# Kernel tuning notes

Hardware: AMD Instinct MI355X
Metric: run time of the kernel (lower is better)

The kernel has to match this reference:

```python
import jax, jax.numpy as jnp
import numpy as np

B, S, H = 2, 2048, 2048
NH, HD = 16, 128


def rotate_half(x):
    x1, x2 = x[..., : x.shape[-1] // 2], x[..., x.shape[-1] // 2 :]
    return jnp.concatenate((-x2, x1), axis=-1)


def setup_inputs() -> dict:
    key = jax.random.key(0)
    ks = jax.random.split(key, 8)
    return {
        "hidden": jax.random.normal(ks[0], (B, S, H), dtype=jnp.float32),
        "cos": jax.random.uniform(ks[1], (S, HD), dtype=jnp.float32),
        "sin": jax.random.uniform(ks[2], (S, HD), dtype=jnp.float32),
        "attention_mask": jnp.zeros((B, 1, S, S), dtype=jnp.float32),
        "Wq": jax.random.normal(ks[3], (H, H), dtype=jnp.float32) * 0.02,
        "Wk": jax.random.normal(ks[4], (H, H), dtype=jnp.float32) * 0.02,
        "Wv": jax.random.normal(ks[5], (H, H), dtype=jnp.float32) * 0.02,
        "Wo": jax.random.normal(ks[6], (H, H), dtype=jnp.float32) * 0.02,
    }


def reference(hidden, cos, sin, attention_mask, Wq, Wk, Wv, Wo):
    b, s, h = hidden.shape
    # torch Linear: y = x @ W.T ; reshape to [B, NH, S, HD]
    def proj(W):
        return (hidden @ W.T).reshape(b, s, NH, HD).transpose(0, 2, 1, 3)

    q, k, v = proj(Wq), proj(Wk), proj(Wv)
    c = cos[None, None, :, :]  # [1,1,S,HD]
    si = sin[None, None, :, :]
    q = q * c + rotate_half(q) * si
    k = k * c + rotate_half(k) * si
    scores = jnp.einsum("bhqd,bhkd->bhqk", q, k) / jnp.sqrt(jnp.float32(HD))
    scores = scores + attention_mask
    attn = jax.nn.softmax(scores.astype(jnp.float32), axis=-1).astype(q.dtype)
    out = jnp.einsum("bhqk,bhkd->bhqd", attn, v)
    out = out.transpose(0, 2, 1, 3).reshape(b, s, h)
    return out @ Wo.T
```

## Files before the change

### kernel.cpp

```cpp
#include <hip/hip_runtime.h>
#include <hip/hip_bf16.h>
#include <math.h>

#define SEQ 2048
#define HID 2048
#define NHEAD 16
#define HDIM 128
#define LDK 4096

typedef __bf16 bf16_t;
typedef __bf16 bf16x2 __attribute__((ext_vector_type(2)));
typedef __bf16 bf16x4_t __attribute__((ext_vector_type(4)));
typedef __bf16 bf16x8 __attribute__((ext_vector_type(8)));
typedef float f32x4 __attribute__((ext_vector_type(4)));
typedef float f32x16 __attribute__((ext_vector_type(16)));
typedef unsigned u32x4 __attribute__((ext_vector_type(4)));

#define MFMA16(a, b, c) __builtin_amdgcn_mfma_f32_16x16x32_bf16(a, b, c, 0, 0, 0)
#define MFMA32(a, b, c) __builtin_amdgcn_mfma_f32_32x32x16_bf16(a, b, c, 0, 0, 0)
#define GLOAD_LDS(g, l) \
  __builtin_amdgcn_global_load_lds((const __attribute__((address_space(1))) void*)(g), \
                                   (__attribute__((address_space(3))) void*)(l), 16, 0, 0)

static __device__ inline unsigned pk2(float lo, float hi) {
  bf16x2 t; t[0] = (bf16_t)lo; t[1] = (bf16_t)hi;
  return __builtin_bit_cast(unsigned, t);
}

static __device__ inline bf16x8 pack_slice(const float* p, int hi) {
  unsigned A1 = pk2(p[0], p[1]);
  unsigned A2 = pk2(p[2], p[3]);
  unsigned B1 = pk2(p[4], p[5]);
  unsigned B2 = pk2(p[6], p[7]);
  unsigned A1s = __shfl_xor(A1, 32, 64);
  unsigned A2s = __shfl_xor(A2, 32, 64);
  unsigned B1s = __shfl_xor(B1, 32, 64);
  unsigned B2s = __shfl_xor(B2, 32, 64);
  unsigned w0 = hi ? B1s : A1;
  unsigned w1 = hi ? B2s : A2;
  unsigned w2 = hi ? B1 : A1s;
  unsigned w3 = hi ? B2 : A2s;
  u32x4 W = {w0, w1, w2, w3};
  return __builtin_bit_cast(bf16x8, W);
}

__global__ void cast_hidden(const float* __restrict__ in, bf16_t* __restrict__ out) {
  int i = blockIdx.x * 256 + threadIdx.x;
  float4 v = ((const float4*)in)[i];
  bf16x4_t b;
  b[0] = (bf16_t)v.x; b[1] = (bf16_t)v.y; b[2] = (bf16_t)v.z; b[3] = (bf16_t)v.w;
  ((bf16x4_t*)out)[i] = b;
}

__global__ void cast_weights(const float* __restrict__ a, const float* __restrict__ b,
                             const float* __restrict__ c, const float* __restrict__ d,
                             bf16_t* __restrict__ out) {
  const float* srcs[4] = {a, b, c, d};
  const float* src = srcs[blockIdx.y];
  bf16_t* dst = out + (size_t)blockIdx.y * (HID * HID);
  int i = blockIdx.x * 256 + threadIdx.x;
  float4 v = ((const float4*)src)[i];
  bf16x4_t o;
  o[0] = (bf16_t)v.x; o[1] = (bf16_t)v.y; o[2] = (bf16_t)v.z; o[3] = (bf16_t)v.w;
  ((bf16x4_t*)dst)[i] = o;
}

__global__ __launch_bounds__(512, 2) void gemm256(
    const bf16_t* __restrict__ A, const bf16_t* __restrict__ Bw,
    bf16_t* __restrict__ Cb, float* __restrict__ Cf, int M, int N, int K) {
  __shared__ char smem[131072];
  const int tid = threadIdx.x, lane = tid & 63, wid = tid >> 6;
  const int wr = wid >> 2, wc = wid & 3;
  const int lr = lane & 15, lg = lane >> 4;
  const int xcd = blockIdx.x & 7, l = blockIdx.x >> 3;
  const int brow = (xcd >> 2) * 8 + (l >> 2);
  const int bcol = (xcd & 3) * 4 + (l & 3);
  const int NT = K >> 6;

  const bf16_t* Ab = A + (size_t)(brow * 256) * K;
  const bf16_t* Bb = Bw + (size_t)(bcol * 256) * K;

  f32x4 acc[8][4] = {};
  bf16x8 af[4], bfr[4];
  const int swz = (lg ^ ((lr >> 1) & 3)) << 4;

#define STAGE_HALF(t_, op, kh)                                                        \
  {                                                                                   \
    int tt = (t_) < NT ? (t_) : NT - 1;                                               \
    const bf16_t* gsrc = (op) ? Bb : Ab;                                              \
    char* ldst = smem + (tt & 1) * 65536 + (op) * 32768 + (kh) * 16384;               \
    _Pragma("unroll") for (int is = 0; is < 2; ++is) {                                \
      int p = tid + is * 512;                                                         \
      int row = p >> 2, ch = p & 3;                                                   \
      GLOAD_LDS(gsrc + (size_t)row * K + tt * 64 + (kh) * 32 +                        \
                    ((ch ^ ((row >> 1) & 3)) * 8),                                    \
                ldst + p * 16);                                                       \
    }                                                                                 \
  }

#define PHASE(cb, kh, mh, LOADB, STAGECALL, VM)                                       \
  {                                                                                   \
    _Pragma("unroll") for (int mf = 0; mf < 4; ++mf) {                                \
      int row = wr * 128 + (mh) * 64 + mf * 16 + lr;                                  \
      af[mf] = *(const bf16x8*)(smem + (cb) * 65536 + (kh) * 16384 + row * 64 + swz); \
    }                                                                                 \
    if (LOADB) {                                                                      \
      _Pragma("unroll") for (int nf = 0; nf < 4; ++nf) {                              \
        int row = wc * 64 + nf * 16 + lr;                                             \
        bfr[nf] = *(const bf16x8*)(smem + (cb) * 65536 + 32768 + (kh) * 16384 +       \
                                   row * 64 + swz);                                   \
      }                                                                               \
    }                                                                                 \
    STAGECALL;                                                                        \
    __builtin_amdgcn_s_barrier();                                                     \
    asm volatile("s_waitcnt lgkmcnt(0)" ::: "memory");                                \
    __builtin_amdgcn_sched_barrier(0);                                                \
    __builtin_amdgcn_s_setprio(1);                                                    \
    _Pragma("unroll") for (int mf = 0; mf < 4; ++mf)                                  \
      _Pragma("unroll") for (int nf = 0; nf < 4; ++nf)                                \
        acc[(mh) * 4 + mf][nf] = MFMA16(af[mf], bfr[nf], acc[(mh) * 4 + mf][nf]);     \
    __builtin_amdgcn_s_setprio(0);                                                    \
    if (VM) { asm volatile("s_waitcnt vmcnt(6)" ::: "memory"); }                      \
    __builtin_amdgcn_s_barrier();                                                     \
    __builtin_amdgcn_sched_barrier(0);                                                \
  }

  STAGE_HALF(0, 1, 0); STAGE_HALF(0, 0, 0); STAGE_HALF(0, 1, 1); STAGE_HALF(0, 0, 1);
  STAGE_HALF(1, 1, 0); STAGE_HALF(1, 0, 0); STAGE_HALF(1, 1, 1);
  asm volatile("s_waitcnt vmcnt(6)" ::: "memory");
  __builtin_amdgcn_s_barrier();
  __builtin_amdgcn_sched_barrier(0);

  const int NI = NT >> 1;
  for (int i = 0; i < NI; ++i) {
    const int t2 = 2 * i;
    PHASE(0, 0, 0, 1, STAGE_HALF(t2 + 1, 0, 1), 0);
    PHASE(0, 0, 1, 0, STAGE_HALF(t2 + 2, 1, 0), 0);
    PHASE(0, 1, 0, 1, STAGE_HALF(t2 + 2, 0, 0), 0);
    PHASE(0, 1, 1, 0, STAGE_HALF(t2 + 2, 1, 1), 1);
    PHASE(1, 0, 0, 1, STAGE_HALF(t2 + 2, 0, 1), 0);
    PHASE(1, 0, 1, 0, STAGE_HALF(t2 + 3, 1, 0), 0);
    PHASE(1, 1, 0, 1, STAGE_HALF(t2 + 3, 0, 0), 0);
    PHASE(1, 1, 1, 0, STAGE_HALF(t2 + 3, 1, 1), 1);
  }
#undef PHASE
#undef STAGE_HALF

#pragma unroll
  for (int mi = 0; mi < 8; ++mi)
#pragma unroll
    for (int nf = 0; nf < 4; ++nf)
#pragma unroll
      for (int r = 0; r < 4; ++r) {
        int row = brow * 256 + wr * 128 + (mi >> 2) * 64 + (mi & 3) * 16 + lg * 4 + r;
        int col = bcol * 256 + wc * 64 + nf * 16 + lr;
        float v = acc[mi][nf][r];
        if (Cf) Cf[(size_t)row * N + col] = v;
        else    Cb[(size_t)row * N + col] = (bf16_t)v;
      }
}

__global__ __launch_bounds__(256, 3) void gemm_bt(
    const bf16_t* __restrict__ A, const bf16_t* __restrict__ Bw,
    bf16_t* __restrict__ Cb, float* __restrict__ Cf,
    int M, int N, int K) {
  __shared__ bf16_t As[2][128 * 32];
  __shared__ bf16_t Bs[2][128 * 32];
  const int tid = threadIdx.x;
  const int lane = tid & 63, wid = tid >> 6;
  const int wr = wid >> 1, wc = wid & 1;
  const int lr = lane & 15, lg = lane >> 4;
  const int nwg = gridDim.x;
  const int lid = (blockIdx.x & 7) * (nwg >> 3) + (blockIdx.x >> 3);
  const int nbc = N >> 7;
  const int brow = lid / nbc, bcol = lid % nbc;

  f32x4 acc[4][4] = {};
  const int swz = lg ^ ((lr >> 1) & 3);

  const int srow = tid >> 2, sch = tid & 3;
#define GSTAGE(k0, bb)                                                                   \
  {                                                                                      \
    _Pragma("unroll") for (int is = 0; is < 2; ++is) {                                   \
      int row = srow + is * 64;                                                          \
      int g = (sch ^ ((row >> 1) & 3)) * 8;                                              \
      GLOAD_LDS(A + (size_t)(brow * 128 + row) * K + (k0) + g,                           \
                &As[bb][(row * 4 + sch) * 8]);                                           \
      GLOAD_LDS(Bw + (size_t)(bcol * 128 + row) * K + (k0) + g,                          \
                &Bs[bb][(row * 4 + sch) * 8]);                                           \
    }                                                                                    \
  }

  GSTAGE(0, 0);
  __syncthreads();

  const int nt = K / 32;
  for (int t = 0; t < nt; ++t) {
    const int cb = t & 1;
    if (t + 1 < nt) GSTAGE((t + 1) * 32, cb ^ 1);
    bf16x8 af[4], bfr[4];
#pragma unroll
    for (int m = 0; m < 4; ++m)
      af[m] = *(const bf16x8*)(&As[cb][(wr * 64 + m * 16 + lr) * 32 + swz * 8]);
#pragma unroll
    for (int n = 0; n < 4; ++n)
      bfr[n] = *(const bf16x8*)(&Bs[cb][(wc * 64 + n * 16 + lr) * 32 + swz * 8]);
#pragma unroll
    for (int m = 0; m < 4; ++m)
#pragma unroll
      for (int n = 0; n < 4; ++n)
        acc[m][n] = MFMA16(af[m], bfr[n], acc[m][n]);
    __syncthreads();
  }
#undef GSTAGE

#pragma unroll
  for (int m = 0; m < 4; ++m)
#pragma unroll
    for (int n = 0; n < 4; ++n)
#pragma unroll
      for (int r = 0; r < 4; ++r) {
        int row = brow * 128 + wr * 64 + m * 16 + lg * 4 + r;
        int col = bcol * 128 + wc * 64 + n * 16 + lr;
        float v = acc[m][n][r];
        if (Cf) Cf[(size_t)row * N + col] = v;
        else    Cb[(size_t)row * N + col] = (bf16_t)v;
      }
}

__global__ void rope_qk(bf16_t* __restrict__ QK,
                        const float* __restrict__ cost, const float* __restrict__ sint) {
  const float SCALE = 0.08838834764831845f;
  int idx = blockIdx.x * 256 + threadIdx.x;
  int d8 = idx & 7;
  int t = idx >> 3;
  int h = t & 15;
  int row = t >> 4;
  int s = row & (SEQ - 1);
  size_t base = (size_t)row * LDK + h * HDIM;
  const float4* cp = (const float4*)(cost + s * HDIM);
  const float4* sp = (const float4*)(sint + s * HDIM);
  float4 c0a = cp[d8 * 2], c0b = cp[d8 * 2 + 1];
  float4 c1a = cp[16 + d8 * 2], c1b = cp[16 + d8 * 2 + 1];
  float4 s0a = sp[d8 * 2], s0b = sp[d8 * 2 + 1];
  float4 s1a = sp[16 + d8 * 2], s1b = sp[16 + d8 * 2 + 1];
  float c0[8] = {c0a.x, c0a.y, c0a.z, c0a.w, c0b.x, c0b.y, c0b.z, c0b.w};
  float c1[8] = {c1a.x, c1a.y, c1a.z, c1a.w, c1b.x, c1b.y, c1b.z, c1b.w};
  float s0[8] = {s0a.x, s0a.y, s0a.z, s0a.w, s0b.x, s0b.y, s0b.z, s0b.w};
  float s1[8] = {s1a.x, s1a.y, s1a.z, s1a.w, s1b.x, s1b.y, s1b.z, s1b.w};

  bf16_t* Q = QK;
  bf16_t* K = QK + 2048;
  bf16x8 qlo = *(bf16x8*)(Q + base + d8 * 8);
  bf16x8 qhi = *(bf16x8*)(Q + base + 64 + d8 * 8);
  bf16x8 klo = *(bf16x8*)(K + base + d8 * 8);
  bf16x8 khi = *(bf16x8*)(K + base + 64 + d8 * 8);
  bf16x8 qlo2, qhi2, klo2, khi2;
#pragma unroll
  for (int j = 0; j < 8; ++j) {
    float q0 = (float)qlo[j], q1 = (float)qhi[j];
    qlo2[j] = (bf16_t)((q0 * c0[j] - q1 * s0[j]) * SCALE);
    qhi2[j] = (bf16_t)((q1 * c1[j] + q0 * s1[j]) * SCALE);
    float k0 = (float)klo[j], k1 = (float)khi[j];
    klo2[j] = (bf16_t)(k0 * c0[j] - k1 * s0[j]);
    khi2[j] = (bf16_t)(k1 * c1[j] + k0 * s1[j]);
  }
  *(bf16x8*)(Q + base + d8 * 8) = qlo2;
  *(bf16x8*)(Q + base + 64 + d8 * 8) = qhi2;
  *(bf16x8*)(K + base + d8 * 8) = klo2;
  *(bf16x8*)(K + base + 64 + d8 * 8) = khi2;
}

__global__ void transpose_v(const bf16_t* __restrict__ Vf, bf16_t* __restrict__ Vt) {
  __shared__ bf16_t t[32][33];
  int tx = threadIdx.x & 31, ty = threadIdx.x >> 5;
  int r0 = blockIdx.y * 32, c0 = blockIdx.x * 32;
#pragma unroll
  for (int j = 0; j < 4; ++j)
    t[ty + j * 8][tx] = Vf[(size_t)(r0 + ty + j * 8) * HID + c0 + tx];
  __syncthreads();
#pragma unroll
  for (int j = 0; j < 4; ++j) {
    int c = c0 + ty + j * 8;
    int r = r0 + tx;
    int h = c >> 7, d = c & 127, b = r >> 11, s = r & (SEQ - 1);
    Vt[(((size_t)(b * NHEAD + h)) * HDIM + d) * SEQ + s] = t[tx][ty + j * 8];
  }
}

__global__ void mask_pack(const float* __restrict__ m, bf16_t* __restrict__ mp) {
  __shared__ float t[32][33];
  int tx = threadIdx.x & 31, ty = threadIdx.x >> 5;
  int q0 = blockIdx.x * 32, k0 = blockIdx.y * 32;
  const float* mb = m + (size_t)blockIdx.z * SEQ * SEQ;
#pragma unroll
  for (int j = 0; j < 4; ++j)
    t[ty + j * 8][tx] = mb[(size_t)(q0 + ty + j * 8) * SEQ + k0 + tx];
  __syncthreads();
  int r = tx & 15, hi = tx >> 4;
  int kl = (r & 3) + 8 * (r >> 2) + 4 * hi;
  bf16_t* ob = mp + ((size_t)(blockIdx.z * 64 + blockIdx.y) * 2048 + q0) * 32;
#pragma unroll
  for (int j = 0; j < 4; ++j) {
    int qloc = ty + j * 8;
    ob[(size_t)qloc * 32 + tx] = (bf16_t)t[qloc][kl];
  }
}

__global__ __launch_bounds__(256, 1) void flash_fwd(
    const bf16_t* __restrict__ Qf, const bf16_t* __restrict__ Kf,
    const bf16_t* __restrict__ Vt, const bf16_t* __restrict__ maskP,
    bf16_t* __restrict__ AO) {
  __shared__ char smem[131072];
  char* KsB = smem;
  char* VsB = smem + 65536;
  const int tid = threadIdx.x, lane = tid & 63, wid = tid >> 6;
  const int q32 = lane & 31, hi = lane >> 5;

  const int x = blockIdx.x;
  const int bh = x & 31, qt = x >> 5;
  const int b = bh >> 4, h = bh & 15;
  const int qg0 = qt * 256 + wid * 64 + q32;

  bf16x8 qf0[8], qf1[8];
  const bf16_t* qp0 = Qf + (size_t)(b * SEQ + qg0) * LDK + h * HDIM + hi * 8;
  const bf16_t* qp1 = qp0 + (size_t)32 * LDK;
#pragma unroll
  for (int ds = 0; ds < 8; ++ds) {
    qf0[ds] = *(const bf16x8*)(qp0 + ds * 16);
    qf1[ds] = *(const bf16x8*)(qp1 + ds * 16);
  }

  const bf16_t* mQ0 = maskP + (size_t)b * 64 * 65536 + (size_t)qg0 * 32 + hi * 16;
  const bf16_t* mQ1 = mQ0 + 32 * 32;

  float mrun0 = -INFINITY, lpart0 = 0.f;
  float mrun1 = -INFINITY, lpart1 = 0.f;
  f32x16 o0[4] = {}, o1[4] = {};

#define STAGE_KV(kt_, bb)                                                                \
  {                                                                                      \
    const int kb0_ = (kt_) * 128;                                                        \
    _Pragma("unroll") for (int is = 0; is < 8; ++is) {                                   \
      int p = tid + is * 256;                                                            \
      int row = p >> 4, ch = p & 15;                                                     \
      int src = (ch * 16) ^ ((row & 15) << 4);                                           \
      GLOAD_LDS((const char*)(Kf + (size_t)(b * SEQ + kb0_ + row) * LDK + h * HDIM) +    \
                    src,                                                                 \
                KsB + (bb) * 32768 + p * 16);                                            \
      GLOAD_LDS((const char*)(Vt + (size_t)(bh * HDIM + row) * SEQ + kb0_) + src,        \
                VsB + (bb) * 32768 + p * 16);                                            \
    }                                                                                    \
  }

  STAGE_KV(0, 0);
  __syncthreads();

  const int NT = SEQ / 128;
  for (int kt = 0; kt < NT; ++kt) {
    const int cur = kt & 1;
    if (kt + 1 < NT) STAGE_KV(kt + 1, cur ^ 1);

#pragma unroll
    for (int kb = 0; kb < 4; ++kb) {
      const int kg = kt * 4 + kb;
      bf16x8 mk00 = *(const bf16x8*)(mQ0 + (size_t)kg * 65536);
      bf16x8 mk01 = *(const bf16x8*)(mQ0 + (size_t)kg * 65536 + 8);
      bf16x8 mk10 = *(const bf16x8*)(mQ1 + (size_t)kg * 65536);
      bf16x8 mk11 = *(const bf16x8*)(mQ1 + (size_t)kg * 65536 + 8);
      f32x16 s0, s1;
#pragma unroll
      for (int r = 0; r < 8; ++r) {
        s0[r] = (float)mk00[r]; s0[8 + r] = (float)mk01[r];
        s1[r] = (float)mk10[r]; s1[8 + r] = (float)mk11[r];
      }

      const int krow = kb * 32 + q32;
      const int kswz = (krow & 15) << 4;
#pragma unroll
      for (int ds = 0; ds < 8; ++ds) {
        bf16x8 kfr = *(const bf16x8*)(KsB + cur * 32768 + krow * 256 +
                                      ((ds * 32 + hi * 16) ^ kswz));
        s0 = MFMA32(kfr, qf0[ds], s0);
        s1 = MFMA32(kfr, qf1[ds], s1);
      }

      bf16x8 pav00, pav01, pav10, pav11;
      {
        float a0 = fmaxf(fmaxf(s0[0], s0[1]), fmaxf(s0[2], s0[3]));
        float a1 = fmaxf(fmaxf(s0[4], s0[5]), fmaxf(s0[6], s0[7]));
        float a2 = fmaxf(fmaxf(s0[8], s0[9]), fmaxf(s0[10], s0[11]));
        float a3 = fmaxf(fmaxf(s0[12], s0[13]), fmaxf(s0[14], s0[15]));
        float mx = fmaxf(fmaxf(a0, a1), fmaxf(a2, a3));
        mx = fmaxf(mx, __shfl_xor(mx, 32, 64));
        if (!__all(mx <= mrun0 + 8.f)) {
          float mnew = fmaxf(mrun0, mx);
          float corr = __expf(mrun0 - mnew);
          mrun0 = mnew; lpart0 *= corr;
#pragma unroll
          for (int d0 = 0; d0 < 4; ++d0)
#pragma unroll
            for (int r = 0; r < 16; ++r) o0[d0][r] *= corr;
        }
        float p_[16];
#pragma unroll
        for (int r = 0; r < 16; ++r) p_[r] = __expf(s0[r] - mrun0);
        float t0 = (p_[0] + p_[1]) + (p_[2] + p_[3]);
        float t1 = (p_[4] + p_[5]) + (p_[6] + p_[7]);
        float t2 = (p_[8] + p_[9]) + (p_[10] + p_[11]);
        float t3 = (p_[12] + p_[13]) + (p_[14] + p_[15]);
        lpart0 += (t0 + t1) + (t2 + t3);
        pav00 = pack_slice(p_, hi);
        pav01 = pack_slice(p_ + 8, hi);
      }
      {
        float a0 = fmaxf(fmaxf(s1[0], s1[1]), fmaxf(s1[2], s1[3]));
        float a1 = fmaxf(fmaxf(s1[4], s1[5]), fmaxf(s1[6], s1[7]));
        float a2 = fmaxf(fmaxf(s1[8], s1[9]), fmaxf(s1[10], s1[11]));
        float a3 = fmaxf(fmaxf(s1[12], s1[13]), fmaxf(s1[14], s1[15]));
        float mx = fmaxf(fmaxf(a0, a1), fmaxf(a2, a3));
        mx = fmaxf(mx, __shfl_xor(mx, 32, 64));
        if (!__all(mx <= mrun1 + 8.f)) {
          float mnew = fmaxf(mrun1, mx);
          float corr = __expf(mrun1 - mnew);
          mrun1 = mnew; lpart1 *= corr;
#pragma unroll
          for (int d0 = 0; d0 < 4; ++d0)
#pragma unroll
            for (int r = 0; r < 16; ++r) o1[d0][r] *= corr;
        }
        float p_[16];
#pragma unroll
        for (int r = 0; r < 16; ++r) p_[r] = __expf(s1[r] - mrun1);
        float t0 = (p_[0] + p_[1]) + (p_[2] + p_[3]);
        float t1 = (p_[4] + p_[5]) + (p_[6] + p_[7]);
        float t2 = (p_[8] + p_[9]) + (p_[10] + p_[11]);
        float t3 = (p_[12] + p_[13]) + (p_[14] + p_[15]);
        lpart1 += (t0 + t1) + (t2 + t3);
        pav10 = pack_slice(p_, hi);
        pav11 = pack_slice(p_ + 8, hi);
      }

      const int vswzr = q32;
#pragma unroll
      for (int s = 0; s < 2; ++s) {
        const int gs = kb * 2 + s;
        bf16x8 pa0 = s ? pav01 : pav00;
        bf16x8 pa1 = s ? pav11 : pav10;
#pragma unroll
        for (int d0 = 0; d0 < 4; ++d0) {
          int vrow = d0 * 32 + vswzr;
          bf16x8 vf = *(const bf16x8*)(VsB + cur * 32768 + vrow * 256 +
                                       ((gs * 32 + hi * 16) ^ ((vrow & 15) << 4)));
          o0[d0] = MFMA32(vf, pa0, o0[d0]);
          o1[d0] = MFMA32(vf, pa1, o1[d0]);
        }
      }
    }
    __syncthreads();
  }
#undef STAGE_KV

  float l0 = lpart0 + __shfl_xor(lpart0, 32, 64);
  float l1 = lpart1 + __shfl_xor(lpart1, 32, 64);
  float rl0 = 1.f / l0, rl1 = 1.f / l1;
  bf16_t* ao0 = AO + (size_t)(b * SEQ + qg0) * HID + h * HDIM;
  bf16_t* ao1 = ao0 + (size_t)32 * HID;
#pragma unroll
  for (int d0 = 0; d0 < 4; ++d0)
#pragma unroll
    for (int g = 0; g < 4; ++g) {
      int d = d0 * 32 + 8 * g + 4 * hi;
      unsigned lo0 = pk2(o0[d0][4 * g + 0] * rl0, o0[d0][4 * g + 1] * rl0);
      unsigned hi0 = pk2(o0[d0][4 * g + 2] * rl0, o0[d0][4 * g + 3] * rl0);
      *(unsigned*)(ao0 + d) = lo0;
      *(unsigned*)(ao0 + d + 2) = hi0;
      unsigned lo1 = pk2(o1[d0][4 * g + 0] * rl1, o1[d0][4 * g + 1] * rl1);
      unsigned hi1 = pk2(o1[d0][4 * g + 2] * rl1, o1[d0][4 * g + 3] * rl1);
      *(unsigned*)(ao1 + d) = lo1;
      *(unsigned*)(ao1 + d + 2) = hi1;
    }
}

extern "C" void kernel_launch(void* const* d_in, const int* in_sizes, int n_in,
                              void* d_out, int out_size, void* d_ws, size_t ws_size,
                              hipStream_t stream) {
  const float* hidden = (const float*)d_in[0];
  const float* cost   = (const float*)d_in[1];
  const float* sint   = (const float*)d_in[2];
  const float* mask   = (const float*)d_in[3];
  const float* Wq     = (const float*)d_in[4];
  const float* Wk     = (const float*)d_in[5];
  const float* Wv     = (const float*)d_in[6];
  const float* Wo     = (const float*)d_in[7];
  float* out = (float*)d_out;
  char* ws = (char*)d_ws;

  bf16_t* Af    = (bf16_t*)(ws + 0);
  bf16_t* Wqb   = (bf16_t*)(ws + 16777216);
  bf16_t* Wvb   = (bf16_t*)(ws + 33554432);
  bf16_t* Wob   = (bf16_t*)(ws + 41943040);
  bf16_t* QK    = (bf16_t*)(ws + 50331648);
  bf16_t* Vf    = (bf16_t*)(ws + 83886080);
  bf16_t* Vt    = (bf16_t*)(ws + 0);
  bf16_t* maskP = (bf16_t*)(ws + 83886080);
  bf16_t* AO    = (bf16_t*)(ws + 16777216);

  cast_hidden<<<8192, 256, 0, stream>>>(hidden, Af);
  cast_weights<<<dim3(4096, 4), 256, 0, stream>>>(Wq, Wk, Wv, Wo, Wqb);

  gemm256<<<256, 512, 0, stream>>>(Af, Wqb, QK, nullptr, 4096, LDK, HID);
  gemm_bt<<<512, 256, 0, stream>>>(Af, Wvb, Vf, nullptr, 4096, HID, HID);

  rope_qk<<<2048, 256, 0, stream>>>(QK, cost, sint);
  transpose_v<<<dim3(64, 128), 256, 0, stream>>>(Vf, Vt);
  mask_pack<<<dim3(64, 64, 2), 256, 0, stream>>>(mask, maskP);

  flash_fwd<<<256, 256, 0, stream>>>(QK, QK + 2048, Vt, maskP, AO);

  gemm_bt<<<512, 256, 0, stream>>>(AO, Wob, nullptr, out, 4096, HID, HID);
}
```

Measured before the change: 347.2 us.

## Split attention key range in two with partial outputs and combine kernel

Splits each flash-attention block's key range into two halves, doubling the grid to 512 blocks and halving LDS so two blocks can reside per CU. Each half writes unnormalized bf16 partial output plus running max and sum, and a new combine kernel merges them with log-sum-exp rescaling. The V staging layout and swizzle are reworked for the smaller 64-key tile. This adds an extra launch and extra global traffic for the partial outputs, plus some bf16 rounding of unnormalized partials.

```diff
diff --git a/kernel.cpp b/kernel.cpp
--- a/kernel.cpp
+++ b/kernel.cpp
@@ -307,20 +307,21 @@
   }
 }
 
-__global__ __launch_bounds__(256, 1) void flash_fwd(
+__global__ __launch_bounds__(256, 2) void flash_fwd(
     const bf16_t* __restrict__ Qf, const bf16_t* __restrict__ Kf,
     const bf16_t* __restrict__ Vt, const bf16_t* __restrict__ maskP,
-    bf16_t* __restrict__ AO) {
-  __shared__ char smem[131072];
+    bf16_t* __restrict__ Op0, bf16_t* __restrict__ Op1, float2* __restrict__ ml) {
+  __shared__ char smem[65536];
   char* KsB = smem;
-  char* VsB = smem + 65536;
+  char* VsB = smem + 32768;
   const int tid = threadIdx.x, lane = tid & 63, wid = tid >> 6;
   const int q32 = lane & 31, hi = lane >> 5;
 
-  const int x = blockIdx.x;
-  const int bh = x & 31, qt = x >> 5;
+  const int lid = (blockIdx.x & 7) * 64 + (blockIdx.x >> 3);
+  const int bh = lid >> 4, kh = (lid >> 3) & 1, qt = lid & 7;
   const int b = bh >> 4, h = bh & 15;
   const int qg0 = qt * 256 + wid * 64 + q32;
+  const int kbase = kh * 1024;
 
   bf16x8 qf0[8], qf1[8];
   const bf16_t* qp0 = Qf + (size_t)(b * SEQ + qg0) * LDK + h * HDIM + hi * 8;
@@ -340,30 +341,33 @@
 
 #define STAGE_KV(kt_, bb)                                                                \
   {                                                                                      \
-    const int kb0_ = (kt_) * 128;                                                        \
-    _Pragma("unroll") for (int is = 0; is < 8; ++is) {                                   \
+    const int kb0_ = kbase + (kt_) * 64;                                                 \
+    _Pragma("unroll") for (int is = 0; is < 4; ++is) {                                   \
       int p = tid + is * 256;                                                            \
-      int row = p >> 4, ch = p & 15;                                                     \
-      int src = (ch * 16) ^ ((row & 15) << 4);                                           \
-      GLOAD_LDS((const char*)(Kf + (size_t)(b * SEQ + kb0_ + row) * LDK + h * HDIM) +    \
-                    src,                                                                 \
-                KsB + (bb) * 32768 + p * 16);                                            \
-      GLOAD_LDS((const char*)(Vt + (size_t)(bh * HDIM + row) * SEQ + kb0_) + src,        \
-                VsB + (bb) * 32768 + p * 16);                                            \
+      int row = p >> 4, u = (p & 15) ^ (row & 15);                                       \
+      GLOAD_LDS(Kf + (size_t)(b * SEQ + kb0_ + row) * LDK + h * HDIM + u * 8,            \
+                KsB + (bb) * 16384 + p * 16);                                            \
+    }                                                                                    \
+    _Pragma("unroll") for (int is = 0; is < 4; ++is) {                                   \
+      int p = tid + is * 256;                                                            \
+      int row = p >> 4, u = (p & 15) ^ (row & 15);                                       \
+      GLOAD_LDS(Vt + (size_t)(bh * HDIM + 2 * row + (u >> 3)) * SEQ + kb0_ +             \
+                    (u & 7) * 8,                                                         \
+                VsB + (bb) * 16384 + p * 16);                                            \
     }                                                                                    \
   }
 
   STAGE_KV(0, 0);
   __syncthreads();
 
-  const int NT = SEQ / 128;
+  const int NT = 1024 / 64;
   for (int kt = 0; kt < NT; ++kt) {
     const int cur = kt & 1;
     if (kt + 1 < NT) STAGE_KV(kt + 1, cur ^ 1);
 
 #pragma unroll
-    for (int kb = 0; kb < 4; ++kb) {
-      const int kg = kt * 4 + kb;
+    for (int kb = 0; kb < 2; ++kb) {
+      const int kg = kh * 32 + kt * 2 + kb;
       bf16x8 mk00 = *(const bf16x8*)(mQ0 + (size_t)kg * 65536);
       bf16x8 mk01 = *(const bf16x8*)(mQ0 + (size_t)kg * 65536 + 8);
       bf16x8 mk10 = *(const bf16x8*)(mQ1 + (size_t)kg * 65536);
@@ -376,11 +380,11 @@
       }
 
       const int krow = kb * 32 + q32;
-      const int kswz = (krow & 15) << 4;
+      const int kx = krow & 15;
 #pragma unroll
       for (int ds = 0; ds < 8; ++ds) {
-        bf16x8 kfr = *(const bf16x8*)(KsB + cur * 32768 + krow * 256 +
-                                      ((ds * 32 + hi * 16) ^ kswz));
+        bf16x8 kfr = *(const bf16x8*)(KsB + cur * 16384 + krow * 256 +
+                                      (((ds * 2 + hi) ^ kx) << 4));
         s0 = MFMA32(kfr, qf0[ds], s0);
         s1 = MFMA32(kfr, qf1[ds], s1);
       }
@@ -441,7 +445,6 @@
         pav11 = pack_slice(p_ + 8, hi);
       }
 
-      const int vswzr = q32;
 #pragma unroll
       for (int s = 0; s < 2; ++s) {
         const int gs = kb * 2 + s;
@@ -449,9 +452,9 @@
         bf16x8 pa1 = s ? pav11 : pav10;
 #pragma unroll
         for (int d0 = 0; d0 < 4; ++d0) {
-          int vrow = d0 * 32 + vswzr;
-          bf16x8 vf = *(const bf16x8*)(VsB + cur * 32768 + vrow * 256 +
-                                       ((gs * 32 + hi * 16) ^ ((vrow & 15) << 4)));
+          int vrow = d0 * 16 + (q32 >> 1);
+          int slot = (((q32 & 1) << 3) + gs * 2 + hi) ^ (vrow & 15);
+          bf16x8 vf = *(const bf16x8*)(VsB + cur * 16384 + vrow * 256 + slot * 16);
           o0[d0] = MFMA32(vf, pa0, o0[d0]);
           o1[d0] = MFMA32(vf, pa1, o1[d0]);
         }
@@ -463,23 +466,51 @@
 
   float l0 = lpart0 + __shfl_xor(lpart0, 32, 64);
   float l1 = lpart1 + __shfl_xor(lpart1, 32, 64);
-  float rl0 = 1.f / l0, rl1 = 1.f / l1;
-  bf16_t* ao0 = AO + (size_t)(b * SEQ + qg0) * HID + h * HDIM;
+  bf16_t* Op = kh ? Op1 : Op0;
+  bf16_t* ao0 = Op + (size_t)(b * SEQ + qg0) * HID + h * HDIM;
   bf16_t* ao1 = ao0 + (size_t)32 * HID;
 #pragma unroll
   for (int d0 = 0; d0 < 4; ++d0)
 #pragma unroll
     for (int g = 0; g < 4; ++g) {
       int d = d0 * 32 + 8 * g + 4 * hi;
-      unsigned lo0 = pk2(o0[d0][4 * g + 0] * rl0, o0[d0][4 * g + 1] * rl0);
-      unsigned hi0 = pk2(o0[d0][4 * g + 2] * rl0, o0[d0][4 * g + 3] * rl0);
+      unsigned lo0 = pk2(o0[d0][4 * g + 0], o0[d0][4 * g + 1]);
+      unsigned hi0 = pk2(o0[d0][4 * g + 2], o0[d0][4 * g + 3]);
       *(unsigned*)(ao0 + d) = lo0;
       *(unsigned*)(ao0 + d + 2) = hi0;
-      unsigned lo1 = pk2(o1[d0][4 * g + 0] * rl1, o1[d0][4 * g + 1] * rl1);
-      unsigned hi1 = pk2(o1[d0][4 * g + 2] * rl1, o1[d0][4 * g + 3] * rl1);
+      unsigned lo1 = pk2(o1[d0][4 * g + 0], o1[d0][4 * g + 1]);
+      unsigned hi1 = pk2(o1[d0][4 * g + 2], o1[d0][4 * g + 3]);
       *(unsigned*)(ao1 + d) = lo1;
       *(unsigned*)(ao1 + d + 2) = hi1;
     }
+  if (hi == 0) {
+    float2* mlb = ml + ((size_t)(kh * 2 + b) * 16 + h) * 2048;
+    float2 v0; v0.x = mrun0; v0.y = l0;
+    float2 v1; v1.x = mrun1; v1.y = l1;
+    mlb[qg0] = v0;
+    mlb[qg0 + 32] = v1;
+  }
+}
+
+__global__ void combine(const bf16_t* __restrict__ Op0, const bf16_t* __restrict__ Op1,
+                        const float2* __restrict__ ml, bf16_t* __restrict__ AO) {
+  int i8 = blockIdx.x * 256 + threadIdx.x;
+  int row = i8 >> 8;
+  int h = (i8 >> 4) & 15;
+  int b = row >> 11, q = row & 2047;
+  float2 ml0 = ml[((size_t)b * 16 + h) * 2048 + q];
+  float2 ml1 = ml[((size_t)(2 + b) * 16 + h) * 2048 + q];
+  float m = fmaxf(ml0.x, ml1.x);
+  float t0 = __expf(ml0.x - m), t1 = __expf(ml1.x - m);
+  float rl = 1.f / (ml0.y * t0 + ml1.y * t1);
+  float r0 = t0 * rl, r1 = t1 * rl;
+  bf16x8 a = ((const bf16x8*)Op0)[i8];
+  bf16x8 c = ((const bf16x8*)Op1)[i8];
+  bf16x8 o;
+#pragma unroll
+  for (int j = 0; j < 8; ++j)
+    o[j] = (bf16_t)((float)a[j] * r0 + (float)c[j] * r1);
+  ((bf16x8*)AO)[i8] = o;
 }
 
 extern "C" void kernel_launch(void* const* d_in, const int* in_sizes, int n_in,
@@ -504,7 +535,10 @@
   bf16_t* Vf    = (bf16_t*)(ws + 83886080);
   bf16_t* Vt    = (bf16_t*)(ws + 0);
   bf16_t* maskP = (bf16_t*)(ws + 83886080);
-  bf16_t* AO    = (bf16_t*)(ws + 16777216);
+  bf16_t* Op0   = (bf16_t*)(ws + 16777216);
+  bf16_t* Op1   = (bf16_t*)(ws + 100663296);
+  float2* mlb   = (float2*)(ws + 33554432);
+  bf16_t* AO    = Op0;
 
   cast_hidden<<<8192, 256, 0, stream>>>(hidden, Af);
   cast_weights<<<dim3(4096, 4), 256, 0, stream>>>(Wq, Wk, Wv, Wo, Wqb);
@@ -516,7 +550,8 @@
   transpose_v<<<dim3(64, 128), 256, 0, stream>>>(Vf, Vt);
   mask_pack<<<dim3(64, 64, 2), 256, 0, stream>>>(mask, maskP);
 
-  flash_fwd<<<256, 256, 0, stream>>>(QK, QK + 2048, Vt, maskP, AO);
+  flash_fwd<<<512, 256, 0, stream>>>(QK, QK + 2048, Vt, maskP, Op0, Op1, mlb);
+  combine<<<4096, 256, 0, stream>>>(Op0, Op1, mlb, AO);
 
   gemm_bt<<<512, 256, 0, stream>>>(AO, Wob, nullptr, out, 4096, HID, HID);
 }
```

Result: slower. 438.6 us (+26.3%).
